# Performance work log

Measured on AMD Instinct MI355X. Metric: run time of the kernel, lower is better.

The kernel has to match this reference:

```python
import jax, jax.numpy as jnp
import numpy as np

N = 20000   # nodes
E = 40000   # edges
B = 1000    # graphs
F = 32      # num_features
D = 64      # dim


def setup_inputs() -> dict:
    key = jax.random.key(0)
    ks = jax.random.split(key, 16)
    def g(k, shape, scale=0.05):
        return jax.random.normal(k, shape, jnp.float32) * scale
    return dict(
        x=jax.random.normal(ks[0], (N, F), jnp.float32),
        edge_attr=jax.random.uniform(ks[1], (E, 5), jnp.float32),
        edge_index=jax.random.randint(ks[2], (2, E), 0, N),
        batch=jnp.sort(jax.random.randint(ks[3], (N,), 0, B)),
        W0=g(ks[4], (D, F)), b0=jnp.zeros((D,), jnp.float32),
        We1=g(ks[5], (128, 5)), be1=jnp.zeros((128,), jnp.float32),
        We2=g(ks[6], (D * D, 128), 0.01), be2=jnp.zeros((D * D,), jnp.float32),
        b_conv=jnp.zeros((D,), jnp.float32),
        W_ih=g(ks[7], (3 * D, D)), W_hh=g(ks[8], (3 * D, D)),
        b_ih=jnp.zeros((3 * D,), jnp.float32), b_hh=jnp.zeros((3 * D,), jnp.float32),
        W_ihl=g(ks[9], (4 * D, 2 * D)), W_hhl=g(ks[10], (4 * D, D)),
        b_ihl=jnp.zeros((4 * D,), jnp.float32), b_hhl=jnp.zeros((4 * D,), jnp.float32),
        W1=g(ks[11], (D, 2 * D)), b1=jnp.zeros((D,), jnp.float32),
        W2=g(ks[12], (1, D)), b2=jnp.zeros((1,), jnp.float32),
    )


def reference(x, edge_attr, edge_index, batch, W0, b0, We1, be1, We2, be2,
              b_conv, W_ih, W_hh, b_ih, b_hh, W_ihl, W_hhl, b_ihl, b_hhl,
              W1, b1, W2, b2):
    src, dst = edge_index[0], edge_index[1]
    # lin0 + relu
    out = jax.nn.relu(x @ W0.T + b0)            # [N, D]
    h = out                                     # GRU hidden
    # edge-conditioned weights (identical each iteration in the original)
    We = jax.nn.relu(edge_attr @ We1.T + be1) @ We2.T + be2
    We = We.reshape(E, D, D)                    # [E, in, out]
    deg = jnp.maximum(jax.ops.segment_sum(jnp.ones((E,), out.dtype), dst, N), 1.0)[:, None]
    for _ in range(3):
        msg = jnp.einsum('ei,eio->eo', out[src], We)          # [E, D]
        agg = jax.ops.segment_sum(msg, dst, num_segments=N) / deg
        m = jax.nn.relu(agg + b_conv)
        # GRU cell (gate order r, z, n as in torch)
        gi = m @ W_ih.T + b_ih
        gh = h @ W_hh.T + b_hh
        ir, iz, inn = jnp.split(gi, 3, -1)
        hr, hz, hn = jnp.split(gh, 3, -1)
        r = jax.nn.sigmoid(ir + hr)
        z = jax.nn.sigmoid(iz + hz)
        n = jnp.tanh(inn + r * hn)
        h = (1.0 - z) * n + z * h
        out = h
    # Set2Set pooling (3 processing steps), LSTM gate order i, f, g, o
    q_star = jnp.zeros((B, 2 * D), out.dtype)
    hl = jnp.zeros((B, D), out.dtype)
    cl = jnp.zeros((B, D), out.dtype)
    for _ in range(3):
        gates = q_star @ W_ihl.T + b_ihl + hl @ W_hhl.T + b_hhl
        i_, f_, g_, o_ = jnp.split(gates, 4, -1)
        cl = jax.nn.sigmoid(f_) * cl + jax.nn.sigmoid(i_) * jnp.tanh(g_)
        hl = jax.nn.sigmoid(o_) * jnp.tanh(cl)
        q = hl                                               # [B, D]
        e = jnp.sum(out * q[batch], -1)                      # [N]
        emax = jax.ops.segment_max(e, batch, num_segments=B)
        a = jnp.exp(e - emax[batch])
        a = a / jax.ops.segment_sum(a, batch, num_segments=B)[batch]
        r_ = jax.ops.segment_sum(a[:, None] * out, batch, num_segments=B)
        q_star = jnp.concatenate([q, r_], -1)                # [B, 2D]
    y = jax.nn.relu(q_star @ W1.T + b1)
    pred = (y @ W2.T + b2).reshape(-1)                       # [B]
    return pred
```

## Files before the change

kernel.cpp:

```cpp
#include <hip/hip_runtime.h>

#define NN 20000
#define NE 40000
#define NGR 1000
#define KH 2
#define WTF_BIAS 524288

typedef unsigned short u16;
typedef u16 u16x8 __attribute__((ext_vector_type(8)));
typedef __bf16 bf16x8 __attribute__((ext_vector_type(8)));
typedef float f32x4 __attribute__((ext_vector_type(4)));

union U8 { u16x8 u; bf16x8 b; };

__device__ __forceinline__ u16 f2bf(float f) {
    union { float f; unsigned u; } v; v.f = f;
    unsigned r = v.u + 0x7FFF + ((v.u >> 16) & 1);
    return (u16)(r >> 16);
}
__device__ __forceinline__ float bf2f(u16 h) {
    union { unsigned u; float f; } v; v.u = ((unsigned)h) << 16;
    return v.f;
}
__device__ __forceinline__ float sigmoidf(float x) { return 1.f / (1.f + __expf(-x)); }

__global__ __launch_bounds__(256) void k_cnt(const int* __restrict__ ei, int* __restrict__ cnt)
{
    for (int e = blockIdx.x * 256 + threadIdx.x; e < NE; e += gridDim.x * 256)
        atomicAdd(&cnt[ei[NE + e]], 1);
}

__global__ __launch_bounds__(1024) void k_scan(const int* __restrict__ cnt,
                                               int* __restrict__ rowptr)
{
    __shared__ int ps[1024];
    int t = threadIdx.x;
    int base = t * 20;
    int loc[20];
    int s = 0;
#pragma unroll
    for (int i = 0; i < 20; ++i) {
        int idx = base + i;
        loc[i] = s;
        s += (idx < NN) ? cnt[idx] : 0;
    }
    ps[t] = s;
    __syncthreads();
    for (int off = 1; off < 1024; off <<= 1) {
        int v = (t >= off) ? ps[t - off] : 0;
        __syncthreads();
        ps[t] += v;
        __syncthreads();
    }
    int ex = (t > 0) ? ps[t - 1] : 0;
#pragma unroll
    for (int i = 0; i < 20; ++i) {
        int idx = base + i;
        if (idx < NN) rowptr[idx] = ex + loc[i];
    }
    if (t == 1023) rowptr[NN] = ps[1023];
}

__global__ __launch_bounds__(256) void k_scatter(const int* __restrict__ ei,
    const int* __restrict__ rowptr, int* __restrict__ cur,
    int* __restrict__ epos, int* __restrict__ srcs)
{
    for (int e = blockIdx.x * 256 + threadIdx.x; e < NE; e += gridDim.x * 256) {
        int d = ei[NE + e];
        int pos = rowptr[d] + atomicAdd(&cur[d], 1);
        epos[e] = pos;
        srcs[pos] = ei[e];
    }
}

__global__ __launch_bounds__(256) void k_pre(
    const float* __restrict__ x, const float* __restrict__ ea,
    const int* __restrict__ batch, const int* __restrict__ epos,
    const float* __restrict__ W0, const float* __restrict__ b0,
    const float* __restrict__ We1, const float* __restrict__ be1,
    const float* __restrict__ We2, const float* __restrict__ be2,
    const float* __restrict__ W_ih, const float* __restrict__ W_hh,
    const float* __restrict__ W_ihl, const float* __restrict__ W_hhl,
    const float* __restrict__ W1,
    float* __restrict__ h, u16* __restrict__ outb, u16* __restrict__ h1,
    u16* __restrict__ WtF, int* __restrict__ gstart, int* __restrict__ gend,
    u16* __restrict__ WgF,
    float* __restrict__ WTihl, float* __restrict__ WThhl, float* __restrict__ WT1)
{
    const int b = blockIdx.x;
    const int t = threadIdx.x;

    if (b < 64) {
        for (int idx = b * 256 + t; idx < 90112; idx += 64 * 256) {
            int i = idx;
            if (i < 32768) {
                int j = i & 7, lane = (i >> 3) & 63;
                int nt = (i >> 9) & 15, ks = i >> 13;
                int o = nt * 16 + (lane & 15);
                int k = ks * 32 + (lane >> 4) * 8 + j;
                float v;
                if (o < 128)      v = (k < 64) ? W_ih[o * 64 + k] : W_hh[o * 64 + k - 64];
                else if (o < 192) v = (k < 64) ? W_ih[o * 64 + k] : 0.f;
                else              v = (k >= 64) ? W_hh[(o - 64) * 64 + k - 64] : 0.f;
                WgF[i] = f2bf(v);
                continue;
            }
            i -= 32768;
            if (i < 32768) { WTihl[i] = W_ihl[(i % 256) * 128 + i / 256]; continue; }
            i -= 32768;
            if (i < 16384) { WThhl[i] = W_hhl[(i % 256) * 64 + i / 256]; continue; }
            i -= 16384;
            WT1[i] = W1[(i % 64) * 128 + i / 64];
        }
        return;
    }
    if (b < 320) {
        int wv = (b - 64) * 4 + (t >> 6);
        int lane = t & 63;
        float w0r[32];
#pragma unroll
        for (int f = 0; f < 32; ++f) w0r[f] = W0[lane * 32 + f];
        float b0v = b0[lane];
        for (int n = wv; n < NN; n += 1024) {
            float xv = (lane < 32) ? x[n * 32 + lane] : 0.f;
            float acc = b0v;
#pragma unroll
            for (int f = 0; f < 32; ++f) acc += __shfl(xv, f, 64) * w0r[f];
            float rv = fmaxf(acc, 0.f);
            h[n * 64 + lane] = rv;
            outb[n * 64 + lane] = f2bf(rv);
        }
        return;
    }
    if (b < 832) {
        for (int idx = (b - 320) * 256 + t; idx < NE * 128; idx += 512 * 256) {
            int e = idx >> 7, k = idx & 127;
            float acc = be1[k];
#pragma unroll
            for (int j = 0; j < 5; ++j)
                acc += ea[e * 5 + j] * We1[k * 5 + j];
            h1[(size_t)epos[e] * 128 + k] = f2bf(fmaxf(acc, 0.f));
        }
        return;
    }
    if (b < 960) {
        for (int idx = (b - 832) * 256 + t; idx < WTF_BIAS + 4096; idx += 128 * 256) {
            float v;
            if (idx < WTF_BIAS) {
                int j = idx & 7, lane = (idx >> 3) & 63;
                int nt = (idx >> 9) & 3, s4 = (idx >> 11) & 3, ch = idx >> 13;
                int o = nt * 16 + (lane & 15);
                int k = s4 * 32 + (lane >> 4) * 8 + j;
                v = We2[(size_t)(ch * 64 + o) * 128 + k];
            } else {
                int bx = idx - WTF_BIAS;
                int j = bx & 7, lane = (bx >> 3) & 63;
                int nt = (bx >> 9) & 3, sb = bx >> 11;
                int o = nt * 16 + (lane & 15);
                int i = sb * 32 + (lane >> 4) * 8 + j;
                v = be2[i * 64 + o];
            }
            WtF[idx] = f2bf(v);
        }
        return;
    }
    {
        for (int idx = (b - 960) * 256 + t; idx < NN; idx += 32 * 256) {
            int bg = batch[idx];
            if (idx == 0 || batch[idx - 1] != bg) gstart[bg] = idx;
            if (idx == NN - 1 || batch[idx + 1] != bg) gend[bg] = idx + 1;
        }
    }
}

__global__ __launch_bounds__(256, 2) void k_msg(
    const u16* __restrict__ outb, const u16* __restrict__ h1,
    const u16* __restrict__ WtF, const int* __restrict__ srcs,
    u16* __restrict__ pbuf)
{
    __shared__ __align__(8) u16 svT[64 * 260];
    const int t = threadIdx.x;
    const int eb0 = blockIdx.x * 256;
    const int kh = blockIdx.y;
    const int ohc = (int)blockIdx.z * 2;

#pragma unroll
    for (int r = 0; r < 8; ++r) {
        int cid = t + 256 * r;
        int row = cid >> 3, c8 = cid & 7;
        int e = eb0 + row;
        u16x8 v = {};
        if (e < NE) { int s = srcs[e]; v = *(const u16x8*)(outb + (size_t)s * 64 + c8 * 8); }
#pragma unroll
        for (int j = 0; j < 8; ++j)
            svT[(c8 * 8 + j) * 260 + row] = v[j];
    }

    const int lane = t & 63, w = t >> 6, r16 = lane & 15, q = lane >> 4;
    const int w64 = w * 64;

    u16x8 h1r[4][4];
#pragma unroll
    for (int sub = 0; sub < 4; ++sub) {
        int e = eb0 + w64 + sub * 16 + r16;
        if (e >= NE) e = NE - 1;
        const u16* hp = h1 + (size_t)e * 128 + q * 8;
#pragma unroll
        for (int s4 = 0; s4 < 4; ++s4)
            h1r[sub][s4] = *(const u16x8*)(hp + s4 * 32);
    }

    f32x4 acc[4][2];
    const f32x4 z4 = {0.f, 0.f, 0.f, 0.f};
#pragma unroll
    for (int sub = 0; sub < 4; ++sub)
#pragma unroll
        for (int nt = 0; nt < 2; ++nt) acc[sub][nt] = z4;

    U8 bufA[8], bufB[8];
    auto LDC = [&](U8 (&dst)[8], int ch) {
        const u16* p = WtF + (size_t)ch * 8192 + ohc * 512 + lane * 8;
#pragma unroll
        for (int s4 = 0; s4 < 4; ++s4)
#pragma unroll
            for (int nt = 0; nt < 2; ++nt)
                dst[s4 * 2 + nt].u = *(const u16x8*)(p + s4 * 2048 + nt * 512);
    };
    auto STEP = [&](U8 (&bv)[8], int ch) {
        f32x4 P[4][2];
#pragma unroll
        for (int s4 = 0; s4 < 4; ++s4)
#pragma unroll
            for (int sub = 0; sub < 4; ++sub) {
                U8 a; a.u = h1r[sub][s4];
#pragma unroll
                for (int nt = 0; nt < 2; ++nt)
                    P[sub][nt] = __builtin_amdgcn_mfma_f32_16x16x32_bf16(
                        a.b, bv[s4 * 2 + nt].b, (s4 == 0) ? z4 : P[sub][nt], 0, 0, 0);
            }
#pragma unroll
        for (int sub = 0; sub < 4; ++sub) {
            int mb = w64 + sub * 16 + q * 4;
            uint2 rv = *(const uint2*)&svT[ch * 260 + mb];
            union { unsigned u; float f; } c0, c1, c2, c3;
            c0.u = rv.x << 16; c1.u = rv.x & 0xffff0000u;
            c2.u = rv.y << 16; c3.u = rv.y & 0xffff0000u;
#pragma unroll
            for (int nt = 0; nt < 2; ++nt) {
                acc[sub][nt][0] += c0.f * P[sub][nt][0];
                acc[sub][nt][1] += c1.f * P[sub][nt][1];
                acc[sub][nt][2] += c2.f * P[sub][nt][2];
                acc[sub][nt][3] += c3.f * P[sub][nt][3];
            }
        }
    };

    LDC(bufA, kh * 32);
    __syncthreads();

#pragma unroll 1
    for (int cc = 0; cc < 32; cc += 2) {
        const int ch = kh * 32 + cc;
        LDC(bufB, ch + 1);
        STEP(bufA, ch);
        if (cc < 30) LDC(bufA, ch + 2);
        STEP(bufB, ch + 1);
    }

    if (kh == KH - 1) {
        U8 bvb[2][2];
#pragma unroll
        for (int sb = 0; sb < 2; ++sb)
#pragma unroll
            for (int nt = 0; nt < 2; ++nt)
                bvb[sb][nt].u = *(const u16x8*)(WtF + WTF_BIAS +
                                                ((sb * 4 + ohc + nt) * 64 + lane) * 8);
#pragma unroll
        for (int sub = 0; sub < 4; ++sub) {
            int m = w64 + sub * 16 + r16;
#pragma unroll
            for (int sb = 0; sb < 2; ++sb) {
                U8 a;
#pragma unroll
                for (int j = 0; j < 8; ++j)
                    a.u[j] = svT[(sb * 32 + q * 8 + j) * 260 + m];
#pragma unroll
                for (int nt = 0; nt < 2; ++nt)
                    acc[sub][nt] = __builtin_amdgcn_mfma_f32_16x16x32_bf16(
                        a.b, bvb[sb][nt].b, acc[sub][nt], 0, 0, 0);
            }
        }
    }

#pragma unroll
    for (int sub = 0; sub < 4; ++sub) {
#pragma unroll
        for (int r = 0; r < 4; ++r) {
            int e = eb0 + w64 + sub * 16 + q * 4 + r;
            if (e >= NE) continue;
            u16* pp = pbuf + (size_t)e * (KH * 64) + kh * 64 + r16;
#pragma unroll
            for (int nt = 0; nt < 2; ++nt)
                pp[(ohc + nt) * 16] = f2bf(acc[sub][nt][r]);
        }
    }
}

__global__ __launch_bounds__(256) void k_gru(float* __restrict__ h, u16* __restrict__ outb,
    const u16* __restrict__ pbuf, const int* __restrict__ rowptr,
    const float* __restrict__ b_conv, const u16* __restrict__ WgF,
    const float* __restrict__ b_ih, const float* __restrict__ b_hh)
{
    __shared__ __align__(16) u16 zA[64 * 132];
    __shared__ float hS[64 * 65];
    const int t = threadIdx.x;
    const int lane = t & 63, w = t >> 6, r16 = lane & 15, q = lane >> 4;
    const int n0 = blockIdx.x * 64;
    const int w16 = w * 16;
    float bcv = b_conv[lane];

#pragma unroll 1
    for (int p = 0; p < 16; ++p) {
        int n = n0 + w16 + p;
        float m = 0.f, hvv = 0.f;
        if (n < NN) {
            int rs = rowptr[n], re = rowptr[n + 1];
            float v = 0.f;
            const u16* pb = pbuf + (size_t)rs * (KH * 64);
            for (int j = rs; j < re; ++j) {
                v += bf2f(pb[lane]) + bf2f(pb[64 + lane]);
                pb += KH * 64;
            }
            m = fmaxf(v / fmaxf((float)(re - rs), 1.f) + bcv, 0.f);
            hvv = h[n * 64 + lane];
        }
        zA[(w16 + p) * 132 + lane] = f2bf(m);
        zA[(w16 + p) * 132 + 64 + lane] = f2bf(hvv);
        hS[(w16 + p) * 65 + lane] = hvv;
    }

    u16x8 afr[4];
#pragma unroll
    for (int ks = 0; ks < 4; ++ks)
        afr[ks] = *(const u16x8*)&zA[(w16 + r16) * 132 + ks * 32 + q * 8];

    f32x4 acc[16];
    const f32x4 z4 = {0.f, 0.f, 0.f, 0.f};
#pragma unroll
    for (int nt = 0; nt < 16; ++nt) acc[nt] = z4;

    U8 bA[4], bB[4];
    auto LDB = [&](U8* dst, int nt) {
#pragma unroll
        for (int ks = 0; ks < 4; ++ks)
            dst[ks].u = *(const u16x8*)(WgF + ((ks * 16 + nt) * 64 + lane) * 8);
    };
    LDB(bA, 0);
#pragma unroll
    for (int nt = 0; nt < 16; ++nt) {
        U8* cur = (nt & 1) ? bB : bA;
        U8* nxt = (nt & 1) ? bA : bB;
        if (nt < 15) LDB(nxt, nt + 1);
        f32x4 c = acc[nt];
#pragma unroll
        for (int ks = 0; ks < 4; ++ks) {
            U8 a; a.u = afr[ks];
            c = __builtin_amdgcn_mfma_f32_16x16x32_bf16(a.b, cur[ks].b, c, 0, 0, 0);
        }
        acc[nt] = c;
    }

#pragma unroll
    for (int reg = 0; reg < 4; ++reg) {
        int nl = w16 + q * 4 + reg;
        int n = n0 + nl;
        if (n >= NN) continue;
#pragma unroll
        for (int dd = 0; dd < 4; ++dd) {
            int d = dd * 16 + r16;
            float rv = acc[dd][reg]      + b_ih[d]       + b_hh[d];
            float zv = acc[4 + dd][reg]  + b_ih[64 + d]  + b_hh[64 + d];
            float iv = acc[8 + dd][reg]  + b_ih[128 + d];
            float hg = acc[12 + dd][reg] + b_hh[128 + d];
            float rr = sigmoidf(rv), zz = sigmoidf(zv);
            float nn = tanhf(iv + rr * hg);
            float hold = hS[nl * 65 + d];
            float hnew = (1.f - zz) * nn + zz * hold;
            h[n * 64 + d] = hnew;
            outb[n * 64 + d] = f2bf(hnew);
        }
    }
}

__global__ __launch_bounds__(256) void k_s2s(const float* __restrict__ h,
    const int* __restrict__ gstart, const int* __restrict__ gend,
    const float* __restrict__ WTihl, const float* __restrict__ WThhl,
    const float* __restrict__ b_ihl, const float* __restrict__ b_hhl,
    const float* __restrict__ WT1, const float* __restrict__ b1,
    const float* __restrict__ W2, const float* __restrict__ b2,
    float* __restrict__ outp)
{
    __shared__ float qs[128];
    __shared__ float hlL[64], clL[64];
    __shared__ float gt[256];
    __shared__ float sm[4], sl[4], sr[4][64];
    const int g = blockIdx.x;
    const int t = threadIdx.x, w = t >> 6, lane = t & 63;
    const int s = gstart[g], e = gend[g];

    if (t < 128) qs[t] = 0.f;
    if (t < 64) { hlL[t] = 0.f; clL[t] = 0.f; }
    __syncthreads();

    for (int step = 0; step < 3; ++step) {
        float ga = b_ihl[t] + b_hhl[t];
#pragma unroll 4
        for (int j = 0; j < 128; ++j)
            ga += qs[j] * WTihl[j * 256 + t];
#pragma unroll 4
        for (int j = 0; j < 64; ++j)
            ga += hlL[j] * WThhl[j * 256 + t];
        gt[t] = ga;
        __syncthreads();
        if (t < 64) {
            float cv = sigmoidf(gt[64 + t]) * clL[t] + sigmoidf(gt[t]) * tanhf(gt[128 + t]);
            float hn = sigmoidf(gt[192 + t]) * tanhf(cv);
            clL[t] = cv; hlL[t] = hn; qs[t] = hn;
        }
        __syncthreads();
        float qv = hlL[lane];
        float M = -3.4e38f, l = 0.f, r = 0.f;
        for (int n = s + w; n < e; n += 4) {
            float hvv = h[n * 64 + lane];
            float p = hvv * qv;
#pragma unroll
            for (int off = 32; off > 0; off >>= 1) p += __shfl_xor(p, off, 64);
            if (p > M) {
                float sc = __expf(M - p);
                l = l * sc + 1.f;
                r = r * sc + hvv;
                M = p;
            } else {
                float pe = __expf(p - M);
                l += pe;
                r += pe * hvv;
            }
        }
        if (lane == 0) { sm[w] = M; sl[w] = l; }
        sr[w][lane] = r;
        __syncthreads();
        if (w == 0) {
            float Mg = fmaxf(fmaxf(sm[0], sm[1]), fmaxf(sm[2], sm[3]));
            float lg = 0.f, rg = 0.f;
#pragma unroll
            for (int wp = 0; wp < 4; ++wp) {
                float sc = __expf(sm[wp] - Mg);
                lg += sl[wp] * sc;
                rg += sr[wp][lane] * sc;
            }
            float inv = (lg > 0.f) ? 1.f / lg : 0.f;
            qs[64 + lane] = rg * inv;
        }
        __syncthreads();
    }
    float acc = 0.f;
#pragma unroll 4
    for (int j = w * 32; j < w * 32 + 32; ++j)
        acc += qs[j] * WT1[j * 64 + lane];
    sr[w][lane] = acc;
    __syncthreads();
    if (w == 0) {
        float y = sr[0][lane] + sr[1][lane] + sr[2][lane] + sr[3][lane] + b1[lane];
        float pr = fmaxf(y, 0.f) * W2[lane];
#pragma unroll
        for (int off = 32; off > 0; off >>= 1) pr += __shfl_xor(pr, off, 64);
        if (lane == 0) outp[g] = pr + b2[0];
    }
}

extern "C" void kernel_launch(void* const* d_in, const int* in_sizes, int n_in,
                              void* d_out, int out_size, void* d_ws, size_t ws_size,
                              hipStream_t stream)
{
    const float* x      = (const float*)d_in[0];
    const float* ea     = (const float*)d_in[1];
    const int*   ei     = (const int*)d_in[2];
    const int*   batch  = (const int*)d_in[3];
    const float* W0     = (const float*)d_in[4];
    const float* b0     = (const float*)d_in[5];
    const float* We1    = (const float*)d_in[6];
    const float* be1    = (const float*)d_in[7];
    const float* We2    = (const float*)d_in[8];
    const float* be2    = (const float*)d_in[9];
    const float* b_conv = (const float*)d_in[10];
    const float* W_ih   = (const float*)d_in[11];
    const float* W_hh   = (const float*)d_in[12];
    const float* b_ih   = (const float*)d_in[13];
    const float* b_hh   = (const float*)d_in[14];
    const float* W_ihl  = (const float*)d_in[15];
    const float* W_hhl  = (const float*)d_in[16];
    const float* b_ihl  = (const float*)d_in[17];
    const float* b_hhl  = (const float*)d_in[18];
    const float* W1     = (const float*)d_in[19];
    const float* b1     = (const float*)d_in[20];
    const float* W2     = (const float*)d_in[21];
    const float* b2     = (const float*)d_in[22];
    float* outp = (float*)d_out;

    char* ws = (char*)d_ws;
    size_t off = 0;
    auto alloc = [&](size_t bytes) -> char* {
        char* p = ws + off;
        off += (bytes + 255) & ~(size_t)255;
        return p;
    };
    u16*   h1     = (u16*)  alloc((size_t)NE * 128 * 2);
    u16*   WtF    = (u16*)  alloc((WTF_BIAS + 4096) * 2);
    u16*   outb   = (u16*)  alloc((size_t)NN * 64 * 2);
    float* h      = (float*)alloc((size_t)NN * 64 * 4);
    u16*   pbuf   = (u16*)  alloc((size_t)NE * KH * 64 * 2);
    int*   rowptr = (int*)  alloc((NN + 1) * 4);
    int*   epos   = (int*)  alloc(NE * 4);
    int*   srcs   = (int*)  alloc(NE * 4);
    int*   cnt    = (int*)  alloc(NN * 4);
    int*   cur    = (int*)  alloc(NN * 4);
    int*   gstart = (int*)  alloc(NGR * 4);
    int*   gend   = (int*)  alloc(NGR * 4);
    u16*   WgF    = (u16*)  alloc(32768 * 2);
    float* WTihl  = (float*)alloc(32768 * 4);
    float* WThhl  = (float*)alloc(16384 * 4);
    float* WT1    = (float*)alloc(8192 * 4);
    if (off > ws_size) return;

    size_t zspan = (size_t)((char*)(gend + NGR) - (char*)cnt);
    hipMemsetAsync(cnt, 0, zspan, stream);

    k_cnt<<<64, 256, 0, stream>>>(ei, cnt);
    k_scan<<<1, 1024, 0, stream>>>(cnt, rowptr);
    k_scatter<<<64, 256, 0, stream>>>(ei, rowptr, cur, epos, srcs);
    k_pre<<<992, 256, 0, stream>>>(x, ea, batch, epos, W0, b0, We1, be1, We2, be2,
                                   W_ih, W_hh, W_ihl, W_hhl, W1,
                                   h, outb, h1, WtF, gstart, gend,
                                   WgF, WTihl, WThhl, WT1);

    dim3 mgrid((NE + 255) / 256, KH, 2);
    for (int it = 0; it < 3; ++it) {
        k_msg<<<mgrid, 256, 0, stream>>>(outb, h1, WtF, srcs, pbuf);
        k_gru<<<313, 256, 0, stream>>>(h, outb, pbuf, rowptr, b_conv,
                                       WgF, b_ih, b_hh);
    }
    k_s2s<<<NGR, 256, 0, stream>>>(h, gstart, gend, WTihl, WThhl, b_ihl, b_hhl,
                                   WT1, b1, W2, b2, outp);
}
```

Measured before the change: 442.1 us.

## Halve k_msg edge tile, software-pipeline MFMA and scaling, swizzle shared memory

Each k_msg block now covers 128 edges instead of 256, which doubles the grid and lowers per-thread register use so launch bounds can allow 3 blocks per SIMD. The per-chunk MFMA products and the scaling by gathered node features are split into two stages and software-pipelined, so the MFMAs for the next chunk are issued before the current chunk is scaled. The transposed shared-memory tile uses an XOR swizzle to reduce bank conflicts. The cost is that every block re-reads the WtF weights, so total weight traffic doubles.

```diff
diff --git a/kernel.cpp b/kernel.cpp
--- a/kernel.cpp
+++ b/kernel.cpp
@@ -173,36 +173,37 @@
     }
 }
 
-__global__ __launch_bounds__(256, 2) void k_msg(
+__global__ __launch_bounds__(256, 3) void k_msg(
     const u16* __restrict__ outb, const u16* __restrict__ h1,
     const u16* __restrict__ WtF, const int* __restrict__ srcs,
     u16* __restrict__ pbuf)
 {
-    __shared__ __align__(8) u16 svT[64 * 260];
+    __shared__ __align__(8) u16 svT[64 * 132];
     const int t = threadIdx.x;
-    const int eb0 = blockIdx.x * 256;
+    const int eb0 = blockIdx.x * 128;
     const int kh = blockIdx.y;
     const int ohc = (int)blockIdx.z * 2;
 
 #pragma unroll
-    for (int r = 0; r < 8; ++r) {
+    for (int r = 0; r < 4; ++r) {
         int cid = t + 256 * r;
         int row = cid >> 3, c8 = cid & 7;
         int e = eb0 + row;
         u16x8 v = {};
         if (e < NE) { int s = srcs[e]; v = *(const u16x8*)(outb + (size_t)s * 64 + c8 * 8); }
+        int rs = row ^ (c8 << 2);
 #pragma unroll
         for (int j = 0; j < 8; ++j)
-            svT[(c8 * 8 + j) * 260 + row] = v[j];
+            svT[(c8 * 8 + j) * 132 + rs] = v[j];
     }
 
     const int lane = t & 63, w = t >> 6, r16 = lane & 15, q = lane >> 4;
-    const int w64 = w * 64;
-
-    u16x8 h1r[4][4];
-#pragma unroll
-    for (int sub = 0; sub < 4; ++sub) {
-        int e = eb0 + w64 + sub * 16 + r16;
+    const int w32 = w * 32;
+
+    u16x8 h1r[2][4];
+#pragma unroll
+    for (int sub = 0; sub < 2; ++sub) {
+        int e = eb0 + w32 + sub * 16 + r16;
         if (e >= NE) e = NE - 1;
         const u16* hp = h1 + (size_t)e * 128 + q * 8;
 #pragma unroll
@@ -210,13 +211,14 @@
             h1r[sub][s4] = *(const u16x8*)(hp + s4 * 32);
     }
 
-    f32x4 acc[4][2];
+    f32x4 acc[2][2];
     const f32x4 z4 = {0.f, 0.f, 0.f, 0.f};
 #pragma unroll
-    for (int sub = 0; sub < 4; ++sub)
+    for (int sub = 0; sub < 2; ++sub)
 #pragma unroll
         for (int nt = 0; nt < 2; ++nt) acc[sub][nt] = z4;
 
+    f32x4 P0[2][2], P1[2][2];
     U8 bufA[8], bufB[8];
     auto LDC = [&](U8 (&dst)[8], int ch) {
         const u16* p = WtF + (size_t)ch * 8192 + ohc * 512 + lane * 8;
@@ -226,22 +228,24 @@
             for (int nt = 0; nt < 2; ++nt)
                 dst[s4 * 2 + nt].u = *(const u16x8*)(p + s4 * 2048 + nt * 512);
     };
-    auto STEP = [&](U8 (&bv)[8], int ch) {
-        f32x4 P[4][2];
+    auto MF = [&](f32x4 (&P)[2][2], U8 (&bv)[8]) {
 #pragma unroll
         for (int s4 = 0; s4 < 4; ++s4)
 #pragma unroll
-            for (int sub = 0; sub < 4; ++sub) {
+            for (int sub = 0; sub < 2; ++sub) {
                 U8 a; a.u = h1r[sub][s4];
 #pragma unroll
                 for (int nt = 0; nt < 2; ++nt)
                     P[sub][nt] = __builtin_amdgcn_mfma_f32_16x16x32_bf16(
                         a.b, bv[s4 * 2 + nt].b, (s4 == 0) ? z4 : P[sub][nt], 0, 0, 0);
             }
-#pragma unroll
-        for (int sub = 0; sub < 4; ++sub) {
-            int mb = w64 + sub * 16 + q * 4;
-            uint2 rv = *(const uint2*)&svT[ch * 260 + mb];
+    };
+    auto SCALE = [&](f32x4 (&P)[2][2], int ch) {
+        int swz = ((ch >> 3) & 7) << 2;
+#pragma unroll
+        for (int sub = 0; sub < 2; ++sub) {
+            int mb = (w32 + sub * 16 + q * 4) ^ swz;
+            uint2 rv = *(const uint2*)&svT[ch * 132 + mb];
             union { unsigned u; float f; } c0, c1, c2, c3;
             c0.u = rv.x << 16; c1.u = rv.x & 0xffff0000u;
             c2.u = rv.y << 16; c3.u = rv.y & 0xffff0000u;
@@ -257,15 +261,22 @@
 
     LDC(bufA, kh * 32);
     __syncthreads();
+    LDC(bufB, kh * 32 + 1);
+    MF(P0, bufA);
 
 #pragma unroll 1
-    for (int cc = 0; cc < 32; cc += 2) {
+    for (int cc = 0; cc < 30; cc += 2) {
         const int ch = kh * 32 + cc;
-        LDC(bufB, ch + 1);
-        STEP(bufA, ch);
-        if (cc < 30) LDC(bufA, ch + 2);
-        STEP(bufB, ch + 1);
-    }
+        LDC(bufA, ch + 2);
+        MF(P1, bufB);
+        SCALE(P0, ch);
+        LDC(bufB, ch + 3);
+        MF(P0, bufA);
+        SCALE(P1, ch + 1);
+    }
+    MF(P1, bufB);
+    SCALE(P0, kh * 32 + 30);
+    SCALE(P1, kh * 32 + 31);
 
     if (kh == KH - 1) {
         U8 bvb[2][2];
@@ -276,14 +287,16 @@
                 bvb[sb][nt].u = *(const u16x8*)(WtF + WTF_BIAS +
                                                 ((sb * 4 + ohc + nt) * 64 + lane) * 8);
 #pragma unroll
-        for (int sub = 0; sub < 4; ++sub) {
-            int m = w64 + sub * 16 + r16;
+        for (int sub = 0; sub < 2; ++sub) {
+            int m = w32 + sub * 16 + r16;
 #pragma unroll
             for (int sb = 0; sb < 2; ++sb) {
                 U8 a;
 #pragma unroll
-                for (int j = 0; j < 8; ++j)
-                    a.u[j] = svT[(sb * 32 + q * 8 + j) * 260 + m];
+                for (int j = 0; j < 8; ++j) {
+                    int ch = sb * 32 + q * 8 + j;
+                    a.u[j] = svT[ch * 132 + (m ^ (((ch >> 3) & 7) << 2))];
+                }
 #pragma unroll
                 for (int nt = 0; nt < 2; ++nt)
                     acc[sub][nt] = __builtin_amdgcn_mfma_f32_16x16x32_bf16(
@@ -293,10 +306,10 @@
     }
 
 #pragma unroll
-    for (int sub = 0; sub < 4; ++sub) {
+    for (int sub = 0; sub < 2; ++sub) {
 #pragma unroll
         for (int r = 0; r < 4; ++r) {
-            int e = eb0 + w64 + sub * 16 + q * 4 + r;
+            int e = eb0 + w32 + sub * 16 + q * 4 + r;
             if (e >= NE) continue;
             u16* pp = pbuf + (size_t)e * (KH * 64) + kh * 64 + r16;
 #pragma unroll
@@ -543,7 +556,7 @@
                                    h, outb, h1, WtF, gstart, gend,
                                    WgF, WTihl, WThhl, WT1);
 
-    dim3 mgrid((NE + 255) / 256, KH, 2);
+    dim3 mgrid((NE + 127) / 128, KH, 2);
     for (int it = 0; it < 3; ++it) {
         k_msg<<<mgrid, 256, 0, stream>>>(outb, h1, WtF, srcs, pbuf);
         k_gru<<<313, 256, 0, stream>>>(h, outb, pbuf, rowptr, b_conv,
```

New measurement: 432.9 us. 2.1% less time.
